# Optimization experiments

Hardware: AMD Instinct MI355X
Metric: run time of the kernel (lower is better)

## Reference

```python
import jax, jax.numpy as jnp
import numpy as np

B, DIN, DOUT = 4096, 4096, 4096

def setup_inputs() -> dict:
    key = jax.random.key(0)
    k1, k2, k3 = jax.random.split(key, 3)
    x = jax.random.normal(k1, (B, DIN), dtype=jnp.float32)
    W = jax.random.normal(k2, (DOUT, DIN), dtype=jnp.float32) * 0.01
    alpha = jnp.ones((DOUT, DIN), dtype=jnp.float32) * 0.01
    eta = jnp.asarray(0.1, dtype=jnp.float32)
    bias = jnp.zeros((DOUT,), dtype=jnp.float32)
    return {"x": x, "W": W, "alpha": alpha, "eta": eta, "bias": bias}

def reference(x, W, alpha, eta, bias):
    # y_slow = x @ W.T + b                          (B, DOUT)
    y_slow = jnp.einsum('bi,oi->bo', x, W) + bias
    # x_norm = x / (||x|| + 1e-8)
    x_norm = x / (jnp.linalg.norm(x, axis=-1, keepdims=True) + 1e-8)
    y_pre = jnp.tanh(y_slow)
    # plastic_i = eta * y_pre_i * sum_j sigmoid(alpha)_ij * x_norm_j * x_j
    # (algebraic rewrite of bmm over per-sample outer-product trace; same math)
    s = jnp.einsum('bi,oi->bo', x_norm * x, jax.nn.sigmoid(alpha))  # (B, DOUT)
    plastic = eta * y_pre * s
    return y_slow + plastic
```

## Files before the change

kernel.cpp:

```cpp
#include <hip/hip_runtime.h>
#include <hip/hip_bf16.h>
#include <math.h>


typedef __attribute__((ext_vector_type(4))) float floatx4;
typedef __attribute__((ext_vector_type(8))) short shortx8;
typedef __attribute__((ext_vector_type(4))) int intx4;

#define MAT_N 4096
#define MAT_ELEMS ((size_t)MAT_N * MAT_N)

__device__ __forceinline__ unsigned short f2bf(float f) {
    unsigned int u = __float_as_uint(f);
    unsigned int r = (u + 0x7fffu + ((u >> 16) & 1u)) >> 16;
    return (unsigned short)r;
}

__device__ __forceinline__ void gload_lds16(const void* gptr, void* lptr) {
    __builtin_amdgcn_global_load_lds(
        (const __attribute__((address_space(1))) unsigned int*)gptr,
        (__attribute__((address_space(3))) unsigned int*)lptr,
        16, 0, 0);
}

__device__ __forceinline__ unsigned lds_off(const void* p) {
    return (unsigned)(unsigned long long)(const __attribute__((address_space(3))) char*)p;
}

template <int OFF>
__device__ __forceinline__ intx4 ldsb128(unsigned addr) {
    intx4 d;
    asm volatile("ds_read_b128 %0, %1 offset:%2" : "=v"(d) : "v"(addr), "i"(OFF));
    return d;
}
template <int OFF>
__device__ __forceinline__ long ldsb64(unsigned addr) {
    long d;
    asm volatile("ds_read_b64 %0, %1 offset:%2" : "=v"(d) : "v"(addr), "i"(OFF));
    return d;
}

#define LGKM0() do { asm volatile("s_waitcnt lgkmcnt(0)" ::: "memory"); \
                     __builtin_amdgcn_sched_barrier(0); } while (0)
#define VMCNT(n) asm volatile("s_waitcnt vmcnt(" #n ")" ::: "memory")
#define BARRIER() do { asm volatile("" ::: "memory"); \
                       __builtin_amdgcn_s_barrier(); \
                       asm volatile("" ::: "memory"); } while (0)

__global__ __launch_bounds__(512) void convx_kernel(const float* __restrict__ x,
                                                    unsigned short* __restrict__ xb,
                                                    unsigned char* __restrict__ p8,
                                                    float* __restrict__ sumsq) {
    size_t base = ((size_t)blockIdx.x * 512 + threadIdx.x) * 8;
    const float4* xp = (const float4*)(x + base);
    float4 a = xp[0], b = xp[1];
    float v[8] = {a.x, a.y, a.z, a.w, b.x, b.y, b.z, b.w};
    shortx8 xo;
    float sq[8];
    float s = 0.f;
#pragma unroll
    for (int j = 0; j < 8; j++) {
        xo[j] = (short)f2bf(v[j]);
        sq[j] = v[j] * v[j];
        s += sq[j];
    }
    *(shortx8*)(xb + base) = xo;
    int p0 = __builtin_amdgcn_cvt_pk_fp8_f32(sq[0], sq[1], 0, false);
    p0 = __builtin_amdgcn_cvt_pk_fp8_f32(sq[2], sq[3], p0, true);
    int p1 = __builtin_amdgcn_cvt_pk_fp8_f32(sq[4], sq[5], 0, false);
    p1 = __builtin_amdgcn_cvt_pk_fp8_f32(sq[6], sq[7], p1, true);
    int2 pv = {p0, p1};
    *(int2*)(p8 + base) = pv;
    for (int off = 32; off > 0; off >>= 1) s += __shfl_down(s, off, 64);
    if ((threadIdx.x & 63) == 0) atomicAdd(&sumsq[base >> 12], s);
}

__global__ __launch_bounds__(512) void convwa_kernel(const float* __restrict__ W,
                                                     const float* __restrict__ alpha,
                                                     unsigned short* __restrict__ wb,
                                                     unsigned char* __restrict__ a8) {
    size_t base = ((size_t)blockIdx.x * 512 + threadIdx.x) * 8;
    const float4* wp = (const float4*)(W + base);
    const float4* ap = (const float4*)(alpha + base);
    float4 w0 = wp[0], w1 = wp[1], a0 = ap[0], a1 = ap[1];
    float wv[8] = {w0.x, w0.y, w0.z, w0.w, w1.x, w1.y, w1.z, w1.w};
    float av[8] = {a0.x, a0.y, a0.z, a0.w, a1.x, a1.y, a1.z, a1.w};
    shortx8 wo;
    float sg[8];
#pragma unroll
    for (int j = 0; j < 8; j++) {
        wo[j] = (short)f2bf(wv[j]);
        sg[j] = 1.0f / (1.0f + __expf(-av[j]));
    }
    *(shortx8*)(wb + base) = wo;
    int p0 = __builtin_amdgcn_cvt_pk_fp8_f32(sg[0], sg[1], 0, false);
    p0 = __builtin_amdgcn_cvt_pk_fp8_f32(sg[2], sg[3], p0, true);
    int p1 = __builtin_amdgcn_cvt_pk_fp8_f32(sg[4], sg[5], 0, false);
    p1 = __builtin_amdgcn_cvt_pk_fp8_f32(sg[6], sg[7], p1, true);
    int2 pv = {p0, p1};
    *(int2*)(a8 + base) = pv;
}

__global__ __launch_bounds__(512, 2) void fused_gemm_kernel(
    const unsigned short* __restrict__ X,
    const unsigned short* __restrict__ Wb,
    const unsigned char* __restrict__ P8,
    const unsigned char* __restrict__ A8,
    const float* __restrict__ bias,
    const float* __restrict__ eta_p,
    const float* __restrict__ sumsq,
    float* __restrict__ out) {
    constexpr int K = MAT_N;
    constexpr int N = MAT_N;
    __shared__ __align__(16) unsigned short sX[2][256 * 64];
    __shared__ __align__(16) unsigned short sW[2][128 * 64];
    __shared__ __align__(16) unsigned char  sP[2][256 * 64];
    __shared__ __align__(16) unsigned char  sA[2][128 * 64];

    const int tid = threadIdx.x;
    const int row0 = blockIdx.y * 256;
    const int col0 = blockIdx.x * 128;
    const int lane = tid & 63;
    const int wave = tid >> 6;
    const int wm = (wave >> 1) * 64;
    const int wn = (wave & 1) * 64;
    const int quad = lane >> 4;
    const int l16 = lane & 15;

    floatx4 accY[4][4], accS[4][4];
#pragma unroll
    for (int i = 0; i < 4; i++)
#pragma unroll
        for (int j = 0; j < 4; j++) {
            accY[i][j] = (floatx4){0.f, 0.f, 0.f, 0.f};
            accS[i][j] = (floatx4){0.f, 0.f, 0.f, 0.f};
        }

    const int rs  = tid >> 3;
    const int kcg = (tid & 7) ^ (rs & 7);
    const size_t xrow = (size_t)(row0 + rs) * K + (size_t)kcg * 8;
    const size_t wrow = (size_t)(col0 + rs) * K + (size_t)kcg * 8;
    const int r8 = tid >> 2;
    const int s8 = (2 * (tid & 3)) ^ (r8 & 6);
    const size_t prow = (size_t)(row0 + r8) * K + (size_t)s8 * 8;
    const size_t arow = (size_t)(col0 + r8) * K + (size_t)s8 * 8;

    const unsigned sx0 = lds_off(&sX[0][0]);
    const unsigned sw0 = lds_off(&sW[0][0]);
    const unsigned sp0 = lds_off(&sP[0][0]);
    const unsigned sa0 = lds_off(&sA[0][0]);

#define PF_X(SEG, BUF, KP) gload_lds16(X + xrow + (size_t)(SEG) * 64 * K + (KP), &sX[BUF][(SEG) * 4096 + tid * 8])
#define PF_W(SEG, BUF, KP) gload_lds16(Wb + wrow + (size_t)(SEG) * 64 * K + (KP), &sW[BUF][(SEG) * 4096 + tid * 8])
#define PF_P(SEG, BUF, KP) gload_lds16(P8 + prow + (size_t)(SEG) * 128 * K + (KP), &sP[BUF][(SEG) * 8192 + tid * 16])
#define PF_A8(BUF, KP)     gload_lds16(A8 + arow + (KP), &sA[BUF][tid * 16])

    PF_X(0, 0, 0); PF_X(1, 0, 0); PF_X(2, 0, 0); PF_X(3, 0, 0);
    PF_W(0, 0, 0); PF_W(1, 0, 0);
    PF_P(0, 0, 0); PF_P(1, 0, 0); PF_A8(0, 0);
    VMCNT(3);
    BARRIER();

    for (int t = 0; t < 64; ++t) {
        const int cur = t & 1;
        const int nx = cur ^ 1;
        const size_t kp = (size_t)((t + 1) & 63) * 64;
        const unsigned sxc = sx0 + (unsigned)cur * (256 * 64 * 2);
        const unsigned swc = sw0 + (unsigned)cur * (128 * 64 * 2);
        const unsigned spc = sp0 + (unsigned)cur * (256 * 64);
        const unsigned sac = sa0 + (unsigned)cur * (128 * 64);

        {
            const unsigned kcp = (unsigned)(((0 * 4 + quad) ^ (l16 & 7)) * 16);
            const unsigned ax = sxc + (unsigned)(wm + l16) * 128 + kcp;
            const unsigned bx = swc + (unsigned)(wn + l16) * 128 + kcp;
            intx4 a[4], b[4];
            a[0] = ldsb128<0>(ax); a[1] = ldsb128<2048>(ax);
            a[2] = ldsb128<4096>(ax); a[3] = ldsb128<6144>(ax);
            b[0] = ldsb128<0>(bx); b[1] = ldsb128<2048>(bx);
            b[2] = ldsb128<4096>(bx); b[3] = ldsb128<6144>(bx);
            PF_X(0, nx, kp); PF_X(1, nx, kp); PF_X(2, nx, kp);
            LGKM0();
            __builtin_amdgcn_s_setprio(1);
#pragma unroll
            for (int i = 0; i < 4; ++i)
#pragma unroll
                for (int j = 0; j < 4; ++j)
                    accY[i][j] = __builtin_amdgcn_mfma_f32_16x16x32_bf16(
                        __builtin_bit_cast(shortx8, a[i]),
                        __builtin_bit_cast(shortx8, b[j]), accY[i][j], 0, 0, 0);
            __builtin_amdgcn_s_setprio(0);
        }
        {
            const unsigned kcp = (unsigned)(((1 * 4 + quad) ^ (l16 & 7)) * 16);
            const unsigned ax = sxc + (unsigned)(wm + l16) * 128 + kcp;
            const unsigned bx = swc + (unsigned)(wn + l16) * 128 + kcp;
            intx4 a[4], b[4];
            a[0] = ldsb128<0>(ax); a[1] = ldsb128<2048>(ax);
            a[2] = ldsb128<4096>(ax); a[3] = ldsb128<6144>(ax);
            b[0] = ldsb128<0>(bx); b[1] = ldsb128<2048>(bx);
            b[2] = ldsb128<4096>(bx); b[3] = ldsb128<6144>(bx);
            PF_X(3, nx, kp); PF_W(0, nx, kp); PF_W(1, nx, kp);
            LGKM0();
            __builtin_amdgcn_s_setprio(1);
#pragma unroll
            for (int i = 0; i < 4; ++i)
#pragma unroll
                for (int j = 0; j < 4; ++j)
                    accY[i][j] = __builtin_amdgcn_mfma_f32_16x16x32_bf16(
                        __builtin_bit_cast(shortx8, a[i]),
                        __builtin_bit_cast(shortx8, b[j]), accY[i][j], 0, 0, 0);
            __builtin_amdgcn_s_setprio(0);
            VMCNT(6);
            BARRIER();
        }
        {
            const unsigned lsp0 = (unsigned)(((0 * 4 + quad) ^ (l16 & 6)) * 8);
            const unsigned lsp1 = (unsigned)(((1 * 4 + quad) ^ (l16 & 6)) * 8);
            const unsigned pxb = spc + (unsigned)(wm + l16) * 64;
            const unsigned qxb = sac + (unsigned)(wn + l16) * 64;
            long p0[4], q0[4], p1[4], q1[4];
            {
                const unsigned px0 = pxb + lsp0;
                p0[0] = ldsb64<0>(px0); p0[1] = ldsb64<1024>(px0);
                p0[2] = ldsb64<2048>(px0); p0[3] = ldsb64<3072>(px0);
            }
            {
                const unsigned qx0 = qxb + lsp0;
                q0[0] = ldsb64<0>(qx0); q0[1] = ldsb64<1024>(qx0);
                q0[2] = ldsb64<2048>(qx0); q0[3] = ldsb64<3072>(qx0);
            }
            {
                const unsigned px1 = pxb + lsp1;
                p1[0] = ldsb64<0>(px1); p1[1] = ldsb64<1024>(px1);
                p1[2] = ldsb64<2048>(px1); p1[3] = ldsb64<3072>(px1);
            }
            {
                const unsigned qx1 = qxb + lsp1;
                q1[0] = ldsb64<0>(qx1); q1[1] = ldsb64<1024>(qx1);
                q1[2] = ldsb64<2048>(qx1); q1[3] = ldsb64<3072>(qx1);
            }
            PF_P(0, nx, kp); PF_P(1, nx, kp); PF_A8(nx, kp);
            LGKM0();
            __builtin_amdgcn_s_setprio(1);
#pragma unroll
            for (int i = 0; i < 4; ++i)
#pragma unroll
                for (int j = 0; j < 4; ++j)
                    accS[i][j] = __builtin_amdgcn_mfma_f32_16x16x32_fp8_fp8(
                        p0[i], q0[j], accS[i][j], 0, 0, 0);
#pragma unroll
            for (int i = 0; i < 4; ++i)
#pragma unroll
                for (int j = 0; j < 4; ++j)
                    accS[i][j] = __builtin_amdgcn_mfma_f32_16x16x32_fp8_fp8(
                        p1[i], q1[j], accS[i][j], 0, 0, 0);
            __builtin_amdgcn_s_setprio(0);
            VMCNT(3);
            BARRIER();
        }
    }
    VMCNT(0);

    const float eta = *eta_p;
#pragma unroll
    for (int i = 0; i < 4; i++) {
#pragma unroll
        for (int r = 0; r < 4; r++) {
            const int grow = row0 + wm + i * 16 + quad * 4 + r;
            const float invn = 1.0f / (sqrtf(sumsq[grow]) + 1e-8f);
#pragma unroll
            for (int j = 0; j < 4; j++) {
                const int gcol = col0 + wn + j * 16 + l16;
                float y = accY[i][j][r] + bias[gcol];
                float s = accS[i][j][r] * invn;
                out[(size_t)grow * N + gcol] = y + eta * tanhf(y) * s;
            }
        }
    }
}

extern "C" void kernel_launch(void* const* d_in, const int* in_sizes, int n_in,
                              void* d_out, int out_size, void* d_ws, size_t ws_size,
                              hipStream_t stream) {
    const float* x     = (const float*)d_in[0];
    const float* W     = (const float*)d_in[1];
    const float* alpha = (const float*)d_in[2];
    const float* eta   = (const float*)d_in[3];
    const float* bias  = (const float*)d_in[4];
    float* out = (float*)d_out;

    char* ws = (char*)d_ws;
    float* sumsq = (float*)ws;
    unsigned short* xb = (unsigned short*)(ws + 16384);
    unsigned short* wb = xb + MAT_ELEMS;
    unsigned char*  p8 = (unsigned char*)(wb + MAT_ELEMS);
    unsigned char*  a8 = p8 + MAT_ELEMS;

    hipMemsetAsync(sumsq, 0, MAT_N * sizeof(float), stream);
    convx_kernel<<<MAT_ELEMS / (8 * 512), 512, 0, stream>>>(x, xb, p8, sumsq);
    convwa_kernel<<<MAT_ELEMS / (8 * 512), 512, 0, stream>>>(W, alpha, wb, a8);

    dim3 grid(MAT_N / 128, MAT_N / 256);
    fused_gemm_kernel<<<grid, 512, 0, stream>>>(xb, wb, p8, a8, bias, eta, sumsq, out);
}
```

Before: 418.4 us.

## Merge conversion kernels, swizzle GEMM tile order, widen fp8 LDS reads

The two conversion kernels are merged into one launch, with the block index selecting the x path or the W/alpha path, which saves one launch and its tail. The GEMM block index is remapped with a swizzle so that concurrently running blocks share row and column tiles in L2. The fp8 LDS reads are changed from eight 64-bit reads per operand to four 128-bit reads, with the swizzle offset adjusted so both k-halves come from one contiguous 16-byte load, and the MFMAs are interleaved per accumulator. This relies on the new LDS addressing matching the existing store layout.

```diff
diff --git a/kernel.cpp b/kernel.cpp
--- a/kernel.cpp
+++ b/kernel.cpp
@@ -6,6 +6,7 @@
 typedef __attribute__((ext_vector_type(4))) float floatx4;
 typedef __attribute__((ext_vector_type(8))) short shortx8;
 typedef __attribute__((ext_vector_type(4))) int intx4;
+typedef __attribute__((ext_vector_type(2))) long longx2;
 
 #define MAT_N 4096
 #define MAT_ELEMS ((size_t)MAT_N * MAT_N)
@@ -31,12 +32,6 @@
 __device__ __forceinline__ intx4 ldsb128(unsigned addr) {
     intx4 d;
     asm volatile("ds_read_b128 %0, %1 offset:%2" : "=v"(d) : "v"(addr), "i"(OFF));
-    return d;
-}
-template <int OFF>
-__device__ __forceinline__ long ldsb64(unsigned addr) {
-    long d;
-    asm volatile("ds_read_b64 %0, %1 offset:%2" : "=v"(d) : "v"(addr), "i"(OFF));
     return d;
 }
 
@@ -47,58 +42,61 @@
                        __builtin_amdgcn_s_barrier(); \
                        asm volatile("" ::: "memory"); } while (0)
 
-__global__ __launch_bounds__(512) void convx_kernel(const float* __restrict__ x,
-                                                    unsigned short* __restrict__ xb,
-                                                    unsigned char* __restrict__ p8,
-                                                    float* __restrict__ sumsq) {
-    size_t base = ((size_t)blockIdx.x * 512 + threadIdx.x) * 8;
-    const float4* xp = (const float4*)(x + base);
-    float4 a = xp[0], b = xp[1];
-    float v[8] = {a.x, a.y, a.z, a.w, b.x, b.y, b.z, b.w};
-    shortx8 xo;
-    float sq[8];
-    float s = 0.f;
-#pragma unroll
-    for (int j = 0; j < 8; j++) {
-        xo[j] = (short)f2bf(v[j]);
-        sq[j] = v[j] * v[j];
-        s += sq[j];
+__global__ __launch_bounds__(512) void conv_kernel(const float* __restrict__ x,
+                                                   const float* __restrict__ W,
+                                                   const float* __restrict__ alpha,
+                                                   unsigned short* __restrict__ xb,
+                                                   unsigned char* __restrict__ p8,
+                                                   unsigned short* __restrict__ wb,
+                                                   unsigned char* __restrict__ a8,
+                                                   float* __restrict__ sumsq) {
+    int bid = blockIdx.x;
+    if (bid < 4096) {
+        size_t base = ((size_t)bid * 512 + threadIdx.x) * 8;
+        const float4* xp = (const float4*)(x + base);
+        float4 a = xp[0], b = xp[1];
+        float v[8] = {a.x, a.y, a.z, a.w, b.x, b.y, b.z, b.w};
+        shortx8 xo;
+        float sq[8];
+        float s = 0.f;
+#pragma unroll
+        for (int j = 0; j < 8; j++) {
+            xo[j] = (short)f2bf(v[j]);
+            sq[j] = v[j] * v[j];
+            s += sq[j];
+        }
+        *(shortx8*)(xb + base) = xo;
+        int p0 = __builtin_amdgcn_cvt_pk_fp8_f32(sq[0], sq[1], 0, false);
+        p0 = __builtin_amdgcn_cvt_pk_fp8_f32(sq[2], sq[3], p0, true);
+        int p1 = __builtin_amdgcn_cvt_pk_fp8_f32(sq[4], sq[5], 0, false);
+        p1 = __builtin_amdgcn_cvt_pk_fp8_f32(sq[6], sq[7], p1, true);
+        int2 pv = {p0, p1};
+        *(int2*)(p8 + base) = pv;
+        for (int off = 32; off > 0; off >>= 1) s += __shfl_down(s, off, 64);
+        if ((threadIdx.x & 63) == 0) atomicAdd(&sumsq[base >> 12], s);
+    } else {
+        bid -= 4096;
+        size_t base = ((size_t)bid * 512 + threadIdx.x) * 8;
+        const float4* wp = (const float4*)(W + base);
+        const float4* ap = (const float4*)(alpha + base);
+        float4 w0 = wp[0], w1 = wp[1], a0 = ap[0], a1 = ap[1];
+        float wv[8] = {w0.x, w0.y, w0.z, w0.w, w1.x, w1.y, w1.z, w1.w};
+        float av[8] = {a0.x, a0.y, a0.z, a0.w, a1.x, a1.y, a1.z, a1.w};
+        shortx8 wo;
+        float sg[8];
+#pragma unroll
+        for (int j = 0; j < 8; j++) {
+            wo[j] = (short)f2bf(wv[j]);
+            sg[j] = 1.0f / (1.0f + __expf(-av[j]));
+        }
+        *(shortx8*)(wb + base) = wo;
+        int p0 = __builtin_amdgcn_cvt_pk_fp8_f32(sg[0], sg[1], 0, false);
+        p0 = __builtin_amdgcn_cvt_pk_fp8_f32(sg[2], sg[3], p0, true);
+        int p1 = __builtin_amdgcn_cvt_pk_fp8_f32(sg[4], sg[5], 0, false);
+        p1 = __builtin_amdgcn_cvt_pk_fp8_f32(sg[6], sg[7], p1, true);
+        int2 pv = {p0, p1};
+        *(int2*)(a8 + base) = pv;
     }
-    *(shortx8*)(xb + base) = xo;
-    int p0 = __builtin_amdgcn_cvt_pk_fp8_f32(sq[0], sq[1], 0, false);
-    p0 = __builtin_amdgcn_cvt_pk_fp8_f32(sq[2], sq[3], p0, true);
-    int p1 = __builtin_amdgcn_cvt_pk_fp8_f32(sq[4], sq[5], 0, false);
-    p1 = __builtin_amdgcn_cvt_pk_fp8_f32(sq[6], sq[7], p1, true);
-    int2 pv = {p0, p1};
-    *(int2*)(p8 + base) = pv;
-    for (int off = 32; off > 0; off >>= 1) s += __shfl_down(s, off, 64);
-    if ((threadIdx.x & 63) == 0) atomicAdd(&sumsq[base >> 12], s);
-}
-
-__global__ __launch_bounds__(512) void convwa_kernel(const float* __restrict__ W,
-                                                     const float* __restrict__ alpha,
-                                                     unsigned short* __restrict__ wb,
-                                                     unsigned char* __restrict__ a8) {
-    size_t base = ((size_t)blockIdx.x * 512 + threadIdx.x) * 8;
-    const float4* wp = (const float4*)(W + base);
-    const float4* ap = (const float4*)(alpha + base);
-    float4 w0 = wp[0], w1 = wp[1], a0 = ap[0], a1 = ap[1];
-    float wv[8] = {w0.x, w0.y, w0.z, w0.w, w1.x, w1.y, w1.z, w1.w};
-    float av[8] = {a0.x, a0.y, a0.z, a0.w, a1.x, a1.y, a1.z, a1.w};
-    shortx8 wo;
-    float sg[8];
-#pragma unroll
-    for (int j = 0; j < 8; j++) {
-        wo[j] = (short)f2bf(wv[j]);
-        sg[j] = 1.0f / (1.0f + __expf(-av[j]));
-    }
-    *(shortx8*)(wb + base) = wo;
-    int p0 = __builtin_amdgcn_cvt_pk_fp8_f32(sg[0], sg[1], 0, false);
-    p0 = __builtin_amdgcn_cvt_pk_fp8_f32(sg[2], sg[3], p0, true);
-    int p1 = __builtin_amdgcn_cvt_pk_fp8_f32(sg[4], sg[5], 0, false);
-    p1 = __builtin_amdgcn_cvt_pk_fp8_f32(sg[6], sg[7], p1, true);
-    int2 pv = {p0, p1};
-    *(int2*)(a8 + base) = pv;
 }
 
 __global__ __launch_bounds__(512, 2) void fused_gemm_kernel(
@@ -118,8 +116,10 @@
     __shared__ __align__(16) unsigned char  sA[2][128 * 64];
 
     const int tid = threadIdx.x;
-    const int row0 = blockIdx.y * 256;
-    const int col0 = blockIdx.x * 128;
+    const int f = blockIdx.y * 32 + blockIdx.x;
+    const int swz = (f & 7) * 64 + (f >> 3);
+    const int row0 = (swz >> 5) * 256;
+    const int col0 = (swz & 31) * 128;
     const int lane = tid & 63;
     const int wave = tid >> 6;
     const int wm = (wave >> 1) * 64;
@@ -215,46 +215,29 @@
             BARRIER();
         }
         {
-            const unsigned lsp0 = (unsigned)(((0 * 4 + quad) ^ (l16 & 6)) * 8);
-            const unsigned lsp1 = (unsigned)(((1 * 4 + quad) ^ (l16 & 6)) * 8);
-            const unsigned pxb = spc + (unsigned)(wm + l16) * 64;
-            const unsigned qxb = sac + (unsigned)(wn + l16) * 64;
-            long p0[4], q0[4], p1[4], q1[4];
-            {
-                const unsigned px0 = pxb + lsp0;
-                p0[0] = ldsb64<0>(px0); p0[1] = ldsb64<1024>(px0);
-                p0[2] = ldsb64<2048>(px0); p0[3] = ldsb64<3072>(px0);
-            }
-            {
-                const unsigned qx0 = qxb + lsp0;
-                q0[0] = ldsb64<0>(qx0); q0[1] = ldsb64<1024>(qx0);
-                q0[2] = ldsb64<2048>(qx0); q0[3] = ldsb64<3072>(qx0);
-            }
-            {
-                const unsigned px1 = pxb + lsp1;
-                p1[0] = ldsb64<0>(px1); p1[1] = ldsb64<1024>(px1);
-                p1[2] = ldsb64<2048>(px1); p1[3] = ldsb64<3072>(px1);
-            }
-            {
-                const unsigned qx1 = qxb + lsp1;
-                q1[0] = ldsb64<0>(qx1); q1[1] = ldsb64<1024>(qx1);
-                q1[2] = ldsb64<2048>(qx1); q1[3] = ldsb64<3072>(qx1);
-            }
+            const unsigned psw = (unsigned)(((2 * quad) ^ (l16 & 6)) * 8);
+            const unsigned px = spc + (unsigned)(wm + l16) * 64 + psw;
+            const unsigned qx = sac + (unsigned)(wn + l16) * 64 + psw;
+            intx4 p[4], q[4];
+            p[0] = ldsb128<0>(px); p[1] = ldsb128<1024>(px);
+            p[2] = ldsb128<2048>(px); p[3] = ldsb128<3072>(px);
+            q[0] = ldsb128<0>(qx); q[1] = ldsb128<1024>(qx);
+            q[2] = ldsb128<2048>(qx); q[3] = ldsb128<3072>(qx);
             PF_P(0, nx, kp); PF_P(1, nx, kp); PF_A8(nx, kp);
             LGKM0();
             __builtin_amdgcn_s_setprio(1);
 #pragma unroll
-            for (int i = 0; i < 4; ++i)
-#pragma unroll
-                for (int j = 0; j < 4; ++j)
+            for (int i = 0; i < 4; ++i) {
+                const longx2 pv = __builtin_bit_cast(longx2, p[i]);
+#pragma unroll
+                for (int j = 0; j < 4; ++j) {
+                    const longx2 qv = __builtin_bit_cast(longx2, q[j]);
                     accS[i][j] = __builtin_amdgcn_mfma_f32_16x16x32_fp8_fp8(
-                        p0[i], q0[j], accS[i][j], 0, 0, 0);
-#pragma unroll
-            for (int i = 0; i < 4; ++i)
-#pragma unroll
-                for (int j = 0; j < 4; ++j)
+                        pv.x, qv.x, accS[i][j], 0, 0, 0);
                     accS[i][j] = __builtin_amdgcn_mfma_f32_16x16x32_fp8_fp8(
-                        p1[i], q1[j], accS[i][j], 0, 0, 0);
+                        pv.y, qv.y, accS[i][j], 0, 0, 0);
+                }
+            }
             __builtin_amdgcn_s_setprio(0);
             VMCNT(3);
             BARRIER();
@@ -298,8 +281,7 @@
     unsigned char*  a8 = p8 + MAT_ELEMS;
 
     hipMemsetAsync(sumsq, 0, MAT_N * sizeof(float), stream);
-    convx_kernel<<<MAT_ELEMS / (8 * 512), 512, 0, stream>>>(x, xb, p8, sumsq);
-    convwa_kernel<<<MAT_ELEMS / (8 * 512), 512, 0, stream>>>(W, alpha, wb, a8);
+    conv_kernel<<<8192, 512, 0, stream>>>(x, W, alpha, xb, p8, wb, a8, sumsq);
 
     dim3 grid(MAT_N / 128, MAT_N / 256);
     fused_gemm_kernel<<<grid, 512, 0, stream>>>(xb, wb, p8, a8, bias, eta, sumsq, out);
```

Result: slower. 446.9 us (+6.8%).
